# Kernel optimization log

Hardware: AMD Instinct MI355X
Metric: run time of the kernel (lower is better)

Reference implementation:

```python
import jax, jax.numpy as jnp
import numpy as np


def _cz_ring_sign(n_qubits):
    # Diagonal of the product of CZ(i, (i+1)%n) over the ring; all CZs commute.
    dim = 1 << n_qubits
    bits = (np.arange(dim)[:, None] >> np.arange(n_qubits - 1, -1, -1)) & 1  # qubit 0 = MSB (cirq order)
    parity = np.zeros(dim, dtype=np.int64)
    for i in range(n_qubits):
        parity += bits[:, i] * bits[:, (i + 1) % n_qubits]
    return ((-1.0) ** parity).astype(np.float32)


def _z_sign(n_qubits, qubit_list):
    dim = 1 << n_qubits
    bits = (np.arange(dim)[:, None] >> np.arange(n_qubits - 1, -1, -1)) & 1
    return ((-1.0) ** bits[:, qubit_list].sum(axis=1)).astype(np.float32)


def setup_inputs() -> dict:
    key = jax.random.key(0)
    k1, k2 = jax.random.split(key)
    batch, n_qubits, n_layers = 16384, 8, 2
    inputs = jax.random.normal(k1, (batch, n_qubits), dtype=jnp.float32)
    params = jax.random.normal(k2, (1, n_qubits * n_layers * 2), dtype=jnp.float32) * 0.1
    return {"inputs": inputs, "params": params}


def _simulate(inputs, params):
    batch, n_qubits = inputs.shape
    n_layers = params.shape[1] // (2 * n_qubits)
    dim = 1 << n_qubits
    cdt = jnp.complex64

    # --- initial layer: RX(inputs[q]) |0> = [cos(x/2), -i sin(x/2)] per qubit; build product state ---
    half = 0.5 * inputs
    c, s = jnp.cos(half), jnp.sin(half)
    state = jnp.ones((batch, 1), dtype=cdt)
    for q in range(n_qubits):  # qubit 0 is most-significant axis (cirq ordering)
        vec = jnp.stack([c[:, q].astype(cdt), (-1j) * s[:, q].astype(cdt)], axis=1)  # (B, 2)
        state = (state[:, :, None] * vec[:, None, :]).reshape(batch, -1)

    # --- variational layers ---
    p = params.reshape(n_layers, n_qubits, 2)  # [..., 0]=RY angle, [..., 1]=RZ angle
    cz_sign = jnp.asarray(_cz_ring_sign(n_qubits))
    for l in range(n_layers):
        for q in range(n_qubits):
            th, ph = 0.5 * p[l, q, 0], 0.5 * p[l, q, 1]
            cy, sy = jnp.cos(th).astype(cdt), jnp.sin(th).astype(cdt)
            em = jnp.exp(-1j * ph.astype(cdt))
            ep = jnp.exp(1j * ph.astype(cdt))
            # U = RZ(phi) @ RY(theta), 2x2
            U = jnp.stack([jnp.stack([em * cy, -em * sy]),
                           jnp.stack([ep * sy, ep * cy])])
            st = state.reshape(batch, 1 << q, 2, 1 << (n_qubits - 1 - q))
            state = jnp.einsum('blir,ji->bljr', st, U).reshape(batch, dim)
        state = state * cz_sign  # fused CZ ring (diagonal)

    # --- readouts: <Z0 Z1> and <Z2 ... Z_{n-1}> ---
    probs = jnp.real(state) ** 2 + jnp.imag(state) ** 2  # (B, dim)
    sign_a = jnp.asarray(_z_sign(n_qubits, list(range(2))))
    sign_b = jnp.asarray(_z_sign(n_qubits, list(range(2, n_qubits))))
    exp_a = probs @ sign_a
    exp_b = probs @ sign_b
    return jnp.stack([exp_a, exp_b], axis=1).astype(jnp.float32)  # (B, 2)


def reference(inputs, params):
    return _simulate(inputs, params)
```

## Files before the change

### kernel.cpp

```cpp
#include <hip/hip_runtime.h>
#include <math.h>


__global__ __launch_bounds__(256) void vqc_kernel(const float* __restrict__ inputs,
                                                  const float* __restrict__ params,
                                                  float* __restrict__ out,
                                                  int batch) {
    __shared__ float Us[16 * 8];
    const int tid = threadIdx.x;

    if (tid < 16) {
        const int l = tid >> 3, q = tid & 7;
        const float th = 0.5f * params[l * 16 + q * 2 + 0];
        const float ph = 0.5f * params[l * 16 + q * 2 + 1];
        const float cy = __cosf(th), sy = __sinf(th);
        const float cp = __cosf(ph), sp = __sinf(ph);
        float* u = &Us[tid * 8];
        u[0] =  cp * cy;  u[1] = -sp * cy;
        u[2] = -cp * sy;  u[3] =  sp * sy;
        u[4] =  cp * sy;  u[5] =  sp * sy;
        u[6] =  cp * cy;  u[7] =  sp * cy;
    }
    __syncthreads();

    const int lane = tid & 63;
    const int w = blockIdx.x * 4 + (tid >> 6);
    if (w >= batch) return;

    const float x = inputs[w * 8 + (lane & 7)];
    const float ch = __cosf(0.5f * x), sh = __sinf(0.5f * x);
    float cq[8], sq[8];
#pragma unroll
    for (int q = 0; q < 8; ++q) {
        cq[q] = __shfl(ch, q, 64);
        sq[q] = __shfl(sh, q, 64);
    }

    float sre[4], sim[4];
#pragma unroll
    for (int j = 0; j < 4; ++j) {
        const int b = (lane << 2) | j;
        float r = 1.0f;
#pragma unroll
        for (int q = 0; q < 8; ++q)
            r *= ((b >> (7 - q)) & 1) ? sq[q] : cq[q];
        const int k = __popc(b) & 3;
        sre[j] = (k == 0) ? r : ((k == 2) ? -r : 0.0f);
        sim[j] = (k == 1) ? -r : ((k == 3) ? r : 0.0f);
    }

#pragma unroll
    for (int l = 0; l < 2; ++l) {
#pragma unroll
        for (int q = 0; q < 6; ++q) {
            const float* u = &Us[(l * 8 + q) * 8];
            const int xb = 5 - q;
            const int m = 1 << xb;
            const int myb = (lane >> xb) & 1;
            const float Are = myb ? u[6] : u[0], Aim = myb ? u[7] : u[1];
            const float Bre = myb ? u[4] : u[2], Bim = myb ? u[5] : u[3];
#pragma unroll
            for (int j = 0; j < 4; ++j) {
                const float ore = __shfl_xor(sre[j], m, 64);
                const float oim = __shfl_xor(sim[j], m, 64);
                const float nre = Are * sre[j] - Aim * sim[j] + Bre * ore - Bim * oim;
                const float nim = Are * sim[j] + Aim * sre[j] + Bre * oim + Bim * ore;
                sre[j] = nre; sim[j] = nim;
            }
        }
#pragma unroll
        for (int q = 6; q < 8; ++q) {
            const float* u = &Us[(l * 8 + q) * 8];
            const int m = 1 << (7 - q);
#pragma unroll
            for (int j0 = 0; j0 < 4; ++j0) {
                if (j0 & m) continue;
                const int j1 = j0 | m;
                const float a0r = sre[j0], a0i = sim[j0];
                const float a1r = sre[j1], a1i = sim[j1];
                sre[j0] = u[0] * a0r - u[1] * a0i + u[2] * a1r - u[3] * a1i;
                sim[j0] = u[0] * a0i + u[1] * a0r + u[2] * a1i + u[3] * a1r;
                sre[j1] = u[4] * a0r - u[5] * a0i + u[6] * a1r - u[7] * a1i;
                sim[j1] = u[4] * a0i + u[5] * a0r + u[6] * a1i + u[7] * a1r;
            }
        }
#pragma unroll
        for (int j = 0; j < 4; ++j) {
            const int b = (lane << 2) | j;
            const int rot = ((b << 1) | (b >> 7)) & 255;
            if (__popc(b & rot) & 1) { sre[j] = -sre[j]; sim[j] = -sim[j]; }
        }
    }

    float sa = 0.0f, sb = 0.0f;
#pragma unroll
    for (int j = 0; j < 4; ++j) {
        const int b = (lane << 2) | j;
        const float p = sre[j] * sre[j] + sim[j] * sim[j];
        sa += (((b >> 7) ^ (b >> 6)) & 1) ? -p : p;
        sb += (__popc(b & 0x3F) & 1) ? -p : p;
    }
#pragma unroll
    for (int off = 32; off >= 1; off >>= 1) {
        sa += __shfl_xor(sa, off, 64);
        sb += __shfl_xor(sb, off, 64);
    }
    if (lane == 0) {
        out[w * 2 + 0] = sa;
        out[w * 2 + 1] = sb;
    }
}

extern "C" void kernel_launch(void* const* d_in, const int* in_sizes, int n_in,
                              void* d_out, int out_size, void* d_ws, size_t ws_size,
                              hipStream_t stream) {
    const float* inputs = (const float*)d_in[0];
    const float* params = (const float*)d_in[1];
    float* out = (float*)d_out;
    const int batch = in_sizes[0] / 8;
    const int blocks = (batch + 3) / 4;
    vqc_kernel<<<blocks, 256, 0, stream>>>(inputs, params, out, batch);
}
```

Baseline: 84.82 us.

## Simulate each batch sample with 16 lanes holding 16 amplitudes each

```diff
diff --git a/kernel.cpp b/kernel.cpp
--- a/kernel.cpp
+++ b/kernel.cpp
@@ -24,43 +24,50 @@
     __syncthreads();
 
     const int lane = tid & 63;
-    const int w = blockIdx.x * 4 + (tid >> 6);
+    const int g = lane >> 4;
+    const int r = lane & 15;
+    const int w = blockIdx.x * 16 + (tid >> 6) * 4 + g;
     if (w >= batch) return;
 
-    const float x = inputs[w * 8 + (lane & 7)];
+    const float x = inputs[w * 8 + (r & 7)];
     const float ch = __cosf(0.5f * x), sh = __sinf(0.5f * x);
     float cq[8], sq[8];
 #pragma unroll
     for (int q = 0; q < 8; ++q) {
-        cq[q] = __shfl(ch, q, 64);
-        sq[q] = __shfl(sh, q, 64);
+        cq[q] = __shfl(ch, (g << 4) | q, 64);
+        sq[q] = __shfl(sh, (g << 4) | q, 64);
     }
 
-    float sre[4], sim[4];
+    float lf = 1.0f;
 #pragma unroll
-    for (int j = 0; j < 4; ++j) {
-        const int b = (lane << 2) | j;
-        float r = 1.0f;
+    for (int q = 0; q < 4; ++q)
+        lf *= ((r >> (3 - q)) & 1) ? sq[q] : cq[q];
+    const int pr = __popc(r);
+
+    float sre[16], sim[16];
 #pragma unroll
-        for (int q = 0; q < 8; ++q)
-            r *= ((b >> (7 - q)) & 1) ? sq[q] : cq[q];
-        const int k = __popc(b) & 3;
-        sre[j] = (k == 0) ? r : ((k == 2) ? -r : 0.0f);
-        sim[j] = (k == 1) ? -r : ((k == 3) ? r : 0.0f);
+    for (int j = 0; j < 16; ++j) {
+        float v = lf;
+        v *= (j & 8) ? sq[4] : cq[4];
+        v *= (j & 4) ? sq[5] : cq[5];
+        v *= (j & 2) ? sq[6] : cq[6];
+        v *= (j & 1) ? sq[7] : cq[7];
+        const int k = (pr + __popc(j)) & 3;
+        sre[j] = (k == 0) ? v : ((k == 2) ? -v : 0.0f);
+        sim[j] = (k == 1) ? -v : ((k == 3) ? v : 0.0f);
     }
 
 #pragma unroll
     for (int l = 0; l < 2; ++l) {
 #pragma unroll
-        for (int q = 0; q < 6; ++q) {
+        for (int q = 0; q < 4; ++q) {
             const float* u = &Us[(l * 8 + q) * 8];
-            const int xb = 5 - q;
-            const int m = 1 << xb;
-            const int myb = (lane >> xb) & 1;
+            const int m = 1 << (3 - q);
+            const int myb = (r >> (3 - q)) & 1;
             const float Are = myb ? u[6] : u[0], Aim = myb ? u[7] : u[1];
             const float Bre = myb ? u[4] : u[2], Bim = myb ? u[5] : u[3];
 #pragma unroll
-            for (int j = 0; j < 4; ++j) {
+            for (int j = 0; j < 16; ++j) {
                 const float ore = __shfl_xor(sre[j], m, 64);
                 const float oim = __shfl_xor(sim[j], m, 64);
                 const float nre = Are * sre[j] - Aim * sim[j] + Bre * ore - Bim * oim;
@@ -69,11 +76,11 @@
             }
         }
 #pragma unroll
-        for (int q = 6; q < 8; ++q) {
+        for (int q = 4; q < 8; ++q) {
             const float* u = &Us[(l * 8 + q) * 8];
             const int m = 1 << (7 - q);
 #pragma unroll
-            for (int j0 = 0; j0 < 4; ++j0) {
+            for (int j0 = 0; j0 < 16; ++j0) {
                 if (j0 & m) continue;
                 const int j1 = j0 | m;
                 const float a0r = sre[j0], a0i = sim[j0];
@@ -85,27 +92,28 @@
             }
         }
 #pragma unroll
-        for (int j = 0; j < 4; ++j) {
-            const int b = (lane << 2) | j;
+        for (int j = 0; j < 16; ++j) {
+            const int b = (r << 4) | j;
             const int rot = ((b << 1) | (b >> 7)) & 255;
             if (__popc(b & rot) & 1) { sre[j] = -sre[j]; sim[j] = -sim[j]; }
         }
     }
 
     float sa = 0.0f, sb = 0.0f;
+    const int pr2 = __popc(r & 3);
 #pragma unroll
-    for (int j = 0; j < 4; ++j) {
-        const int b = (lane << 2) | j;
+    for (int j = 0; j < 16; ++j) {
         const float p = sre[j] * sre[j] + sim[j] * sim[j];
-        sa += (((b >> 7) ^ (b >> 6)) & 1) ? -p : p;
-        sb += (__popc(b & 0x3F) & 1) ? -p : p;
+        sa += p;
+        sb += ((pr2 + __popc(j)) & 1) ? -p : p;
     }
+    if (((r >> 3) ^ (r >> 2)) & 1) sa = -sa;
 #pragma unroll
-    for (int off = 32; off >= 1; off >>= 1) {
+    for (int off = 8; off >= 1; off >>= 1) {
         sa += __shfl_xor(sa, off, 64);
         sb += __shfl_xor(sb, off, 64);
     }
-    if (lane == 0) {
+    if (r == 0) {
         out[w * 2 + 0] = sa;
         out[w * 2 + 1] = sb;
     }
@@ -118,6 +126,6 @@
     const float* params = (const float*)d_in[1];
     float* out = (float*)d_out;
     const int batch = in_sizes[0] / 8;
-    const int blocks = (batch + 3) / 4;
+    const int blocks = (batch + 15) / 16;
     vqc_kernel<<<blocks, 256, 0, stream>>>(inputs, params, out, batch);
 }
```

After: 81.02 us. 4.5% less time.
